# Optimization experiments

Measured on AMD Instinct MI355X. Metric: run time of the kernel, lower is better.

The kernel has to match this reference:

```python
import jax, jax.numpy as jnp
import numpy as np
import math

B, S, D = 4, 2048, 1024
H = 1
HD = D // H  # head_dim == hidden_dim since num_heads=1 (required by source's phase_encoder Linear)
HALF = HD // 2
SYNC_LOSS_WEIGHT = 0.01


def setup_inputs() -> dict:
    key = jax.random.key(0)
    ks = jax.random.split(key, 11)
    wstd = 0.02
    inp = {
        "x": jax.random.normal(ks[0], (B, S, D), dtype=jnp.float32),
        "Wq": jax.random.normal(ks[1], (D, D), dtype=jnp.float32) * wstd,
        "bq": jnp.zeros((D,), jnp.float32),
        "Wk": jax.random.normal(ks[2], (D, D), dtype=jnp.float32) * wstd,
        "bk": jnp.zeros((D,), jnp.float32),
        "Wv": jax.random.normal(ks[3], (D, D), dtype=jnp.float32) * wstd,
        "bv": jnp.zeros((D,), jnp.float32),
        "Wp": jax.random.normal(ks[4], (D, D), dtype=jnp.float32) * wstd,
        "bp": jnp.zeros((D,), jnp.float32),
        "Wo": jax.random.normal(ks[5], (D, D), dtype=jnp.float32) * wstd,
        "bo": jnp.zeros((D,), jnp.float32),
        "bifurcation_param": jnp.asarray(1.0, jnp.float32),
        "phase_coupling": jnp.asarray(0.5, jnp.float32),
    }
    return inp


def _phase(t, Wp, bp):
    # t: [B,H,S,HD] -> instantaneous phase via angle(complex(first_half, second_half))
    pf = t @ Wp.T + bp
    re, im = pf[..., :HALF], pf[..., HALF:]
    return jnp.arctan2(im, re)  # [B,H,S,HALF]


def reference(x, Wq, bq, Wk, bk, Wv, bv, Wp, bp, Wo, bo, bifurcation_param, phase_coupling):
    b, s, d = x.shape
    Q = (x @ Wq.T + bq).reshape(b, s, H, HD).transpose(0, 2, 1, 3)  # [B,H,S,HD]
    K = (x @ Wk.T + bk).reshape(b, s, H, HD).transpose(0, 2, 1, 3)
    V = (x @ Wv.T + bv).reshape(b, s, H, HD).transpose(0, 2, 1, 3)

    scores = jnp.einsum("bhqd,bhkd->bhqk", Q, K) / math.sqrt(HD)

    pQ = _phase(Q, Wp, bp)
    pK = _phase(K, Wp, bp)
    # mean_d cos(pQ - pK) == (cos(pQ)@cos(pK)^T + sin(pQ)@sin(pK)^T) / HALF
    sync = (jnp.einsum("bhqd,bhkd->bhqk", jnp.cos(pQ), jnp.cos(pK))
            + jnp.einsum("bhqd,bhkd->bhqk", jnp.sin(pQ), jnp.sin(pK))) / HALF

    t = jnp.tanh(scores)
    bif = bifurcation_param * t * (1.0 - t)

    chaotic = scores + phase_coupling * sync + bif
    attn = jax.nn.softmax(chaotic, axis=-1)

    av = jnp.einsum("bhqk,bhkd->bhqd", attn, V)
    av = av.transpose(0, 2, 1, 3).reshape(b, s, d)
    out = av @ Wo.T + bo

    # torch.var default: unbiased (ddof=1), over last dim of sync
    sync_loss = SYNC_LOSS_WEIGHT * jnp.var(sync, axis=-1, ddof=1).mean()
    return out, sync_loss
```

## Files before the change

### kernel.cpp

```cpp
#include <hip/hip_runtime.h>
#include <hip/hip_bf16.h>
#include <math.h>

#define S_LEN 2048
#define D_MODEL 1024
#define N_BATCH 4
#define N_HALF 512

typedef unsigned short u16;
typedef __attribute__((ext_vector_type(8))) short bf16x8;
typedef __attribute__((ext_vector_type(4))) float f32x4;

__device__ inline u16 f2bf(float v) {
  __hip_bfloat16 h = __float2bfloat16(v);
  return *reinterpret_cast<u16*>(&h);
}
__device__ inline float bf2f(u16 u) {
  __hip_bfloat16 h = *reinterpret_cast<__hip_bfloat16*>(&u);
  return __bfloat162float(h);
}
__device__ inline void gl2lds16(const void* g, void* l) {
  __builtin_amdgcn_global_load_lds(
      (const __attribute__((address_space(1))) unsigned int*)g,
      (__attribute__((address_space(3))) unsigned int*)l, 16, 0, 0);
}
__device__ inline float fast_tanh(float x) {
  float e = __expf(2.0f * x);
  return 1.0f - 2.0f / (e + 1.0f);
}

__global__ __launch_bounds__(256)
void cast_bf4(const float* __restrict__ src, u16* __restrict__ dst, long long n4) {
  long long i = (long long)blockIdx.x * 256 + threadIdx.x;
  if (i >= n4) return;
  float4 v = ((const float4*)src)[i];
  ushort4 o;
  o.x = f2bf(v.x); o.y = f2bf(v.y); o.z = f2bf(v.z); o.w = f2bf(v.w);
  ((ushort4*)dst)[i] = o;
}
__global__ __launch_bounds__(256)
void cast_split(const float* __restrict__ src, u16* __restrict__ hi,
                u16* __restrict__ lo, long long n) {
  long long i = (long long)blockIdx.x * 256 + threadIdx.x;
  if (i < n) {
    float v = src[i];
    u16 h = f2bf(v);
    hi[i] = h;
    lo[i] = f2bf(v - bf2f(h));
  }
}
__global__ __launch_bounds__(256)
void transpose_split(const float* __restrict__ src, u16* __restrict__ hi,
                     u16* __restrict__ lo) {
  __shared__ float t[32][33];
  const int bx = blockIdx.x * 32;
  const int by = blockIdx.y * 32;
  const int c = threadIdx.x & 31;
  const int r0 = (threadIdx.x >> 5) * 4;
#pragma unroll
  for (int r = 0; r < 4; r++)
    t[r0 + r][c] = src[(long long)(by + r0 + r) * D_MODEL + bx + c];
  __syncthreads();
#pragma unroll
  for (int r = 0; r < 4; r++) {
    float v = t[c][r0 + r];
    long long idx = (long long)(bx + r0 + r) * D_MODEL + by + c;
    u16 h = f2bf(v);
    hi[idx] = h;
    lo[idx] = f2bf(v - bf2f(h));
  }
}
__global__ __launch_bounds__(256)
void zero_stats(float* __restrict__ p, int n) {
  int i = blockIdx.x * 256 + threadIdx.x;
  if (i < n) p[i] = 0.f;
}
__global__ __launch_bounds__(256)
void w2_bias(const float* __restrict__ Wo, const float* __restrict__ bv,
             float* __restrict__ w2b) {
  const int d = blockIdx.x;
  const int tid = threadIdx.x;
  float acc = 0.f;
  for (int j = tid; j < D_MODEL; j += 256)
    acc += Wo[(long long)d * D_MODEL + j] * bv[j];
#pragma unroll
  for (int m = 1; m < 64; m <<= 1) acc += __shfl_xor(acc, m);
  __shared__ float red[4];
  if ((tid & 63) == 0) red[tid >> 6] = acc;
  __syncthreads();
  if (tid == 0) w2b[d] = red[0] + red[1] + red[2] + red[3];
}

__global__ __launch_bounds__(256, 2)
void qk_fused(const u16* __restrict__ X, const u16* __restrict__ Wq,
              const u16* __restrict__ Wk,
              const float* __restrict__ bq, const float* __restrict__ bk,
              u16* __restrict__ Qo, u16* __restrict__ Ko) {
  __shared__ u16 Xs[128 * 32];
  __shared__ u16 Qs[128 * 32];
  __shared__ u16 Ks[128 * 32];
  const int tid  = threadIdx.x;
  const int wave = tid >> 6;
  const int lane = tid & 63;
  const int quad = lane >> 4;
  const int tc   = lane & 15;
  const int bm = blockIdx.y * 128;
  const int bn = blockIdx.x * 128;
  const int wm = (wave & 1) * 64;
  const int wn = (wave >> 1) * 64;

  f32x4 acc1[4][4], acc2[4][4];
#pragma unroll
  for (int i = 0; i < 4; i++)
#pragma unroll
    for (int j = 0; j < 4; j++) {
      acc1[i][j] = (f32x4){0.f, 0.f, 0.f, 0.f};
      acc2[i][j] = (f32x4){0.f, 0.f, 0.f, 0.f};
    }

  const int srow = wave * 32 + (lane >> 2);
  const int scol = (lane & 3) * 8;
  const u16* gx = X  + (long long)(bm + srow) * D_MODEL + scol;
  const u16* gq = Wq + (long long)(bn + srow) * D_MODEL + scol;
  const u16* gk = Wk + (long long)(bn + srow) * D_MODEL + scol;
  const int wb = (wave * 32) * 32;
  const long long r16 = 16LL * D_MODEL;

  for (int k0 = 0; k0 < D_MODEL; k0 += 32) {
    gl2lds16(gx,       Xs + wb);
    gl2lds16(gx + r16, Xs + wb + 512);
    gl2lds16(gq,       Qs + wb);
    gl2lds16(gq + r16, Qs + wb + 512);
    gl2lds16(gk,       Ks + wb);
    gl2lds16(gk + r16, Ks + wb + 512);
    gx += 32; gq += 32; gk += 32;
    __syncthreads();
    bf16x8 af[4], bq4[4], bk4[4];
#pragma unroll
    for (int i = 0; i < 4; i++)
      af[i] = *(const bf16x8*)(Xs + (wm + i * 16 + tc) * 32 + quad * 8);
#pragma unroll
    for (int j = 0; j < 4; j++) {
      int o = (wn + j * 16 + tc) * 32 + quad * 8;
      bq4[j] = *(const bf16x8*)(Qs + o);
      bk4[j] = *(const bf16x8*)(Ks + o);
    }
#pragma unroll
    for (int i = 0; i < 4; i++)
#pragma unroll
      for (int j = 0; j < 4; j++) {
        acc1[i][j] = __builtin_amdgcn_mfma_f32_16x16x32_bf16(af[i], bq4[j], acc1[i][j], 0, 0, 0);
        acc2[i][j] = __builtin_amdgcn_mfma_f32_16x16x32_bf16(af[i], bk4[j], acc2[i][j], 0, 0, 0);
      }
    __syncthreads();
  }

#pragma unroll
  for (int i = 0; i < 4; i++) {
    const int row0 = bm + wm + i * 16 + quad * 4;
#pragma unroll
    for (int j = 0; j < 4; j++) {
      const int col = bn + wn + j * 16 + tc;
#pragma unroll
      for (int r = 0; r < 4; r++) {
        long long idx = (long long)(row0 + r) * D_MODEL + col;
        Qo[idx] = f2bf(acc1[i][j][r] + bq[col]);
        Ko[idx] = f2bf(acc2[i][j][r] + bk[col]);
      }
    }
  }
}

__global__ __launch_bounds__(256, 2)
void pf_fused(const u16* __restrict__ Qb, const u16* __restrict__ Wp,
              const float* __restrict__ bp,
              u16* __restrict__ pfQ, u16* __restrict__ pfK,
              long long TDo) {
  __shared__ u16 Qs[128 * 32];
  __shared__ u16 Ks[128 * 32];
  __shared__ u16 Ws[128 * 32];
  const int tid  = threadIdx.x;
  const int wave = tid >> 6;
  const int lane = tid & 63;
  const int quad = lane >> 4;
  const int tc   = lane & 15;
  const int bm = blockIdx.y * 128;
  const int bn = blockIdx.x * 128;
  const int wm = (wave & 1) * 64;
  const int wn = (wave >> 1) * 64;

  f32x4 acc1[4][4], acc2[4][4];
#pragma unroll
  for (int i = 0; i < 4; i++)
#pragma unroll
    for (int j = 0; j < 4; j++) {
      acc1[i][j] = (f32x4){0.f, 0.f, 0.f, 0.f};
      acc2[i][j] = (f32x4){0.f, 0.f, 0.f, 0.f};
    }

  const int srow = wave * 32 + (lane >> 2);
  const int scol = (lane & 3) * 8;
  const u16* gq = Qb + (long long)(bm + srow) * D_MODEL + scol;
  const u16* gk = gq + TDo;
  const u16* gw = Wp + (long long)(bn + srow) * D_MODEL + scol;
  const int wb = (wave * 32) * 32;
  const long long r16 = 16LL * D_MODEL;

  for (int k0 = 0; k0 < D_MODEL; k0 += 32) {
    gl2lds16(gq,       Qs + wb);
    gl2lds16(gq + r16, Qs + wb + 512);
    gl2lds16(gk,       Ks + wb);
    gl2lds16(gk + r16, Ks + wb + 512);
    gl2lds16(gw,       Ws + wb);
    gl2lds16(gw + r16, Ws + wb + 512);
    gq += 32; gk += 32; gw += 32;
    __syncthreads();
    bf16x8 aq[4], ak[4], bw[4];
#pragma unroll
    for (int i = 0; i < 4; i++) {
      int o = (wm + i * 16 + tc) * 32 + quad * 8;
      aq[i] = *(const bf16x8*)(Qs + o);
      ak[i] = *(const bf16x8*)(Ks + o);
    }
#pragma unroll
    for (int j = 0; j < 4; j++)
      bw[j] = *(const bf16x8*)(Ws + (wn + j * 16 + tc) * 32 + quad * 8);
#pragma unroll
    for (int i = 0; i < 4; i++)
#pragma unroll
      for (int j = 0; j < 4; j++) {
        acc1[i][j] = __builtin_amdgcn_mfma_f32_16x16x32_bf16(aq[i], bw[j], acc1[i][j], 0, 0, 0);
        acc2[i][j] = __builtin_amdgcn_mfma_f32_16x16x32_bf16(ak[i], bw[j], acc2[i][j], 0, 0, 0);
      }
    __syncthreads();
  }

#pragma unroll
  for (int i = 0; i < 4; i++) {
    const int row0 = bm + wm + i * 16 + quad * 4;
#pragma unroll
    for (int j = 0; j < 4; j++) {
      const int col = bn + wn + j * 16 + tc;
#pragma unroll
      for (int r = 0; r < 4; r++) {
        long long idx = (long long)(row0 + r) * D_MODEL + col;
        float b = bp[col];
        pfQ[idx] = f2bf(acc1[i][j][r] + b);
        pfK[idx] = f2bf(acc2[i][j][r] + b);
      }
    }
  }
}

__global__ __launch_bounds__(256)
void mfma_gemm_out3(const u16* __restrict__ Ah, const u16* __restrict__ Al,
                    const u16* __restrict__ Bh, const u16* __restrict__ Bl,
                    const float* __restrict__ bias, float* __restrict__ C,
                    int N, int K) {
  __shared__ u16 Ash[128 * 32];
  __shared__ u16 Asl[128 * 32];
  __shared__ u16 Bsh[128 * 32];
  __shared__ u16 Bsl[128 * 32];
  const int tid  = threadIdx.x;
  const int wave = tid >> 6;
  const int lane = tid & 63;
  const int quad = lane >> 4;
  const int tc   = lane & 15;
  const int bm = blockIdx.y * 128;
  const int bn = blockIdx.x * 128;
  const int wm = (wave & 1) * 64;
  const int wn = (wave >> 1) * 64;

  f32x4 acc[4][4];
#pragma unroll
  for (int i = 0; i < 4; i++)
#pragma unroll
    for (int j = 0; j < 4; j++) acc[i][j] = (f32x4){0.f, 0.f, 0.f, 0.f};

  const int srow = wave * 32 + (lane >> 2);
  const int scol = (lane & 3) * 8;
  long long aoff = (long long)(bm + srow) * K + scol;
  long long boff = (long long)(bn + srow) * K + scol;
  const u16 *gah = Ah + aoff, *gal = Al + aoff;
  const u16 *gbh = Bh + boff, *gbl = Bl + boff;
  const int wbase = (wave * 32) * 32;
  const long long r16K = 16LL * K;

  for (int k0 = 0; k0 < K; k0 += 32) {
    gl2lds16(gah,        Ash + wbase);
    gl2lds16(gah + r16K, Ash + wbase + 512);
    gl2lds16(gal,        Asl + wbase);
    gl2lds16(gal + r16K, Asl + wbase + 512);
    gl2lds16(gbh,        Bsh + wbase);
    gl2lds16(gbh + r16K, Bsh + wbase + 512);
    gl2lds16(gbl,        Bsl + wbase);
    gl2lds16(gbl + r16K, Bsl + wbase + 512);
    gah += 32; gal += 32; gbh += 32; gbl += 32;
    __syncthreads();
    bf16x8 ah[4], al[4], bh[4], bl[4];
#pragma unroll
    for (int i = 0; i < 4; i++) {
      int o = (wm + i * 16 + tc) * 32 + quad * 8;
      ah[i] = *(const bf16x8*)(Ash + o);
      al[i] = *(const bf16x8*)(Asl + o);
    }
#pragma unroll
    for (int j = 0; j < 4; j++) {
      int o = (wn + j * 16 + tc) * 32 + quad * 8;
      bh[j] = *(const bf16x8*)(Bsh + o);
      bl[j] = *(const bf16x8*)(Bsl + o);
    }
#pragma unroll
    for (int i = 0; i < 4; i++)
#pragma unroll
      for (int j = 0; j < 4; j++) {
        acc[i][j] = __builtin_amdgcn_mfma_f32_16x16x32_bf16(ah[i], bh[j], acc[i][j], 0, 0, 0);
        acc[i][j] = __builtin_amdgcn_mfma_f32_16x16x32_bf16(ah[i], bl[j], acc[i][j], 0, 0, 0);
        acc[i][j] = __builtin_amdgcn_mfma_f32_16x16x32_bf16(al[i], bh[j], acc[i][j], 0, 0, 0);
      }
    __syncthreads();
  }
#pragma unroll
  for (int i = 0; i < 4; i++) {
    const int row0 = bm + wm + i * 16 + quad * 4;
#pragma unroll
    for (int j = 0; j < 4; j++) {
      const int col = bn + wn + j * 16 + tc;
      float b = bias ? bias[col] : 0.f;
#pragma unroll
      for (int r = 0; r < 4; r++)
        C[(long long)(row0 + r) * N + col] = acc[i][j][r] + b;
    }
  }
}

__global__ __launch_bounds__(256)
void vwt_kernel(const u16* __restrict__ W2h, const u16* __restrict__ W2l,
                const u16* __restrict__ X, const float* __restrict__ w2b,
                u16* __restrict__ Ch, u16* __restrict__ Cl,
                long long sB, long long sC) {
  __shared__ u16 Ah[128 * 32];
  __shared__ u16 Al[128 * 32];
  __shared__ u16 Bs[128 * 32];
  const int tid  = threadIdx.x;
  const int wave = tid >> 6;
  const int lane = tid & 63;
  const int quad = lane >> 4;
  const int tc   = lane & 15;
  const int bm = blockIdx.y * 128;
  const int bn = blockIdx.x * 128;
  const long long z = blockIdx.z;
  const int wm = (wave & 1) * 64;
  const int wn = (wave >> 1) * 64;

  f32x4 acc[4][4];
#pragma unroll
  for (int i = 0; i < 4; i++)
#pragma unroll
    for (int j = 0; j < 4; j++) acc[i][j] = (f32x4){0.f, 0.f, 0.f, 0.f};

  const int srow = wave * 32 + (lane >> 2);
  const int scol = (lane & 3) * 8;
  const long long aoff = (long long)(bm + srow) * D_MODEL + scol;
  const u16* gah = W2h + aoff;
  const u16* gal = W2l + aoff;
  const u16* gb  = X + z * sB + (long long)(bn + srow) * D_MODEL + scol;
  const int wb = (wave * 32) * 32;
  const long long r16 = 16LL * D_MODEL;

  for (int k0 = 0; k0 < D_MODEL; k0 += 32) {
    gl2lds16(gah,       Ah + wb);
    gl2lds16(gah + r16, Ah + wb + 512);
    gl2lds16(gal,       Al + wb);
    gl2lds16(gal + r16, Al + wb + 512);
    gl2lds16(gb,        Bs + wb);
    gl2lds16(gb + r16,  Bs + wb + 512);
    gah += 32; gal += 32; gb += 32;
    __syncthreads();
    bf16x8 ah4[4], al4[4], bx[4];
#pragma unroll
    for (int i = 0; i < 4; i++) {
      int o = (wm + i * 16 + tc) * 32 + quad * 8;
      ah4[i] = *(const bf16x8*)(Ah + o);
      al4[i] = *(const bf16x8*)(Al + o);
    }
#pragma unroll
    for (int j = 0; j < 4; j++)
      bx[j] = *(const bf16x8*)(Bs + (wn + j * 16 + tc) * 32 + quad * 8);
#pragma unroll
    for (int i = 0; i < 4; i++)
#pragma unroll
      for (int j = 0; j < 4; j++) {
        acc[i][j] = __builtin_amdgcn_mfma_f32_16x16x32_bf16(ah4[i], bx[j], acc[i][j], 0, 0, 0);
        acc[i][j] = __builtin_amdgcn_mfma_f32_16x16x32_bf16(al4[i], bx[j], acc[i][j], 0, 0, 0);
      }
    __syncthreads();
  }

  u16* Chz = Ch + z * sC;
  u16* Clz = Cl + z * sC;
#pragma unroll
  for (int i = 0; i < 4; i++) {
    const int row0 = bm + wm + i * 16 + quad * 4;
#pragma unroll
    for (int j = 0; j < 4; j++) {
      const int col = bn + wn + j * 16 + tc;
#pragma unroll
      for (int r = 0; r < 4; r++) {
        float v = acc[i][j][r] + w2b[row0 + r];
        long long idx = (long long)(row0 + r) * S_LEN + col;
        u16 h = f2bf(v);
        Chz[idx] = h;
        Clz[idx] = f2bf(v - bf2f(h));
      }
    }
  }
}

__global__ __launch_bounds__(256)
void gemm_bsplit(const u16* __restrict__ A,
                 const u16* __restrict__ Bh, const u16* __restrict__ Bl,
                 const float* __restrict__ bias, float* __restrict__ C,
                 int N, int K, long long sA, long long sB, long long sC) {
  __shared__ u16 As[128 * 32];
  __shared__ u16 Bsh[128 * 32];
  __shared__ u16 Bsl[128 * 32];
  const int tid  = threadIdx.x;
  const int wave = tid >> 6;
  const int lane = tid & 63;
  const int quad = lane >> 4;
  const int tc   = lane & 15;
  const int bm = blockIdx.y * 128;
  const int bn = blockIdx.x * 128;
  const long long z = blockIdx.z;
  const int wm = (wave & 1) * 64;
  const int wn = (wave >> 1) * 64;

  f32x4 acc[4][4];
#pragma unroll
  for (int i = 0; i < 4; i++)
#pragma unroll
    for (int j = 0; j < 4; j++) acc[i][j] = (f32x4){0.f, 0.f, 0.f, 0.f};

  const int srow = wave * 32 + (lane >> 2);
  const int scol = (lane & 3) * 8;
  const long long boff = (long long)(bn + srow) * K + scol;
  const u16* ga  = A + z * sA + (long long)(bm + srow) * K + scol;
  const u16* gbh = Bh + z * sB + boff;
  const u16* gbl = Bl + z * sB + boff;
  const int wb = (wave * 32) * 32;
  const long long r16K = 16LL * K;

  for (int k0 = 0; k0 < K; k0 += 32) {
    gl2lds16(ga,         As + wb);
    gl2lds16(ga + r16K,  As + wb + 512);
    gl2lds16(gbh,        Bsh + wb);
    gl2lds16(gbh + r16K, Bsh + wb + 512);
    gl2lds16(gbl,        Bsl + wb);
    gl2lds16(gbl + r16K, Bsl + wb + 512);
    ga += 32; gbh += 32; gbl += 32;
    __syncthreads();
    bf16x8 af[4], bh[4], bl[4];
#pragma unroll
    for (int i = 0; i < 4; i++)
      af[i] = *(const bf16x8*)(As + (wm + i * 16 + tc) * 32 + quad * 8);
#pragma unroll
    for (int j = 0; j < 4; j++) {
      int o = (wn + j * 16 + tc) * 32 + quad * 8;
      bh[j] = *(const bf16x8*)(Bsh + o);
      bl[j] = *(const bf16x8*)(Bsl + o);
    }
#pragma unroll
    for (int i = 0; i < 4; i++)
#pragma unroll
      for (int j = 0; j < 4; j++) {
        acc[i][j] = __builtin_amdgcn_mfma_f32_16x16x32_bf16(af[i], bh[j], acc[i][j], 0, 0, 0);
        acc[i][j] = __builtin_amdgcn_mfma_f32_16x16x32_bf16(af[i], bl[j], acc[i][j], 0, 0, 0);
      }
    __syncthreads();
  }

  float* Cz = C + z * sC;
#pragma unroll
  for (int i = 0; i < 4; i++) {
    const int row0 = bm + wm + i * 16 + quad * 4;
#pragma unroll
    for (int j = 0; j < 4; j++) {
      const int col = bn + wn + j * 16 + tc;
#pragma unroll
      for (int r = 0; r < 4; r++)
        Cz[(long long)(row0 + r) * N + col] = acc[i][j][r] + bias[col];
    }
  }
}

__global__ __launch_bounds__(256, 2)
void chaotic_fused(const u16* __restrict__ Q, const u16* __restrict__ Kt,
                   const u16* __restrict__ Uq, const u16* __restrict__ Uk,
                   float* __restrict__ Cc,
                   float* __restrict__ ssum, float* __restrict__ ssq,
                   const float* __restrict__ bifp, const float* __restrict__ pcp) {
  __shared__ u16 Qs[128 * 64];
  __shared__ u16 Ks[128 * 64];
  __shared__ u16 Us[128 * 64];
  __shared__ u16 Ws[128 * 64];
  const int tid  = threadIdx.x;
  const int wave = tid >> 6;
  const int lane = tid & 63;
  const int quad = lane >> 4;
  const int tc   = lane & 15;
  const int bm = blockIdx.y * 128;
  const int bn = blockIdx.x * 128;
  const long long z = blockIdx.z;
  const long long sQ = (long long)S_LEN * D_MODEL;
  const int wm = (wave & 1) * 64;
  const int wn = (wave >> 1) * 64;

  f32x4 acc1[4][4], acc2[4][4];
#pragma unroll
  for (int i = 0; i < 4; i++)
#pragma unroll
    for (int j = 0; j < 4; j++) {
      acc1[i][j] = (f32x4){0.f, 0.f, 0.f, 0.f};
      acc2[i][j] = (f32x4){0.f, 0.f, 0.f, 0.f};
    }

  const int srow8  = lane >> 3;
  const int scol   = ((lane & 7) ^ srow8) * 8;
  const int srowb  = wave * 32;
  const u16* gq = Q  + z * sQ + (long long)(bm + srowb + srow8) * D_MODEL + scol;
  const u16* gk = Kt + z * sQ + (long long)(bn + srowb + srow8) * D_MODEL + scol;
  const u16* gu = Uq + z * sQ + (long long)(bm + srowb + srow8) * D_MODEL + scol;
  const u16* gw = Uk + z * sQ + (long long)(bn + srowb + srow8) * D_MODEL + scol;
  const int wb = srowb * 64;
  const long long r8 = 8LL * D_MODEL;

  const int swzA = tc & 7;

  for (int k0 = 0; k0 < D_MODEL; k0 += 64) {
#pragma unroll
    for (int c = 0; c < 4; c++) {
      gl2lds16(gq + c * r8, Qs + wb + c * 512);
      gl2lds16(gk + c * r8, Ks + wb + c * 512);
      gl2lds16(gu + c * r8, Us + wb + c * 512);
      gl2lds16(gw + c * r8, Ws + wb + c * 512);
    }
    gq += 64; gk += 64; gu += 64; gw += 64;
    __syncthreads();
    {
      bf16x8 af[4][2], bg[4][2];
#pragma unroll
      for (int i = 0; i < 4; i++) {
        const int ra = (wm + i * 16 + tc) * 64;
        const int rb = (wn + i * 16 + tc) * 64;
#pragma unroll
        for (int ks = 0; ks < 2; ks++) {
          const int co = ((ks * 4 + quad) ^ swzA) * 8;
          af[i][ks] = *(const bf16x8*)(Qs + ra + co);
          bg[i][ks] = *(const bf16x8*)(Ks + rb + co);
        }
      }
#pragma unroll
      for (int i = 0; i < 4; i++)
#pragma unroll
        for (int j = 0; j < 4; j++) {
          acc1[i][j] = __builtin_amdgcn_mfma_f32_16x16x32_bf16(af[i][0], bg[j][0], acc1[i][j], 0, 0, 0);
          acc1[i][j] = __builtin_amdgcn_mfma_f32_16x16x32_bf16(af[i][1], bg[j][1], acc1[i][j], 0, 0, 0);
        }
    }
    {
      bf16x8 cf[4][2], dg[4][2];
#pragma unroll
      for (int i = 0; i < 4; i++) {
        const int ra = (wm + i * 16 + tc) * 64;
        const int rb = (wn + i * 16 + tc) * 64;
#pragma unroll
        for (int ks = 0; ks < 2; ks++) {
          const int co = ((ks * 4 + quad) ^ swzA) * 8;
          cf[i][ks] = *(const bf16x8*)(Us + ra + co);
          dg[i][ks] = *(const bf16x8*)(Ws + rb + co);
        }
      }
#pragma unroll
      for (int i = 0; i < 4; i++)
#pragma unroll
        for (int j = 0; j < 4; j++) {
          acc2[i][j] = __builtin_amdgcn_mfma_f32_16x16x32_bf16(cf[i][0], dg[j][0], acc2[i][j], 0, 0, 0);
          acc2[i][j] = __builtin_amdgcn_mfma_f32_16x16x32_bf16(cf[i][1], dg[j][1], acc2[i][j], 0, 0, 0);
        }
    }
    __syncthreads();
  }

  const float bif = *bifp;
  const float pc  = *pcp;
  float rsum[4][4], rsq[4][4];
#pragma unroll
  for (int i = 0; i < 4; i++)
#pragma unroll
    for (int r = 0; r < 4; r++) { rsum[i][r] = 0.f; rsq[i][r] = 0.f; }

  float* C = Cc + z * (long long)S_LEN * S_LEN;
#pragma unroll
  for (int i = 0; i < 4; i++) {
    const int row0 = bm + wm + i * 16 + quad * 4;
#pragma unroll
    for (int j = 0; j < 4; j++) {
      const int col = bn + wn + j * 16 + tc;
#pragma unroll
      for (int r = 0; r < 4; r++) {
        float sc = acc1[i][j][r] * 0.03125f;
        float sy = acc2[i][j][r] * (1.0f / 512.0f);
        float t  = fast_tanh(sc);
        C[(long long)(row0 + r) * S_LEN + col] = sc + pc * sy + bif * t * (1.0f - t);
        rsum[i][r] += sy;
        rsq[i][r]  += sy * sy;
      }
    }
  }
#pragma unroll
  for (int m = 1; m < 16; m <<= 1) {
#pragma unroll
    for (int i = 0; i < 4; i++)
#pragma unroll
      for (int r = 0; r < 4; r++) {
        rsum[i][r] += __shfl_xor(rsum[i][r], m);
        rsq[i][r]  += __shfl_xor(rsq[i][r], m);
      }
  }
  if (tc == 0) {
#pragma unroll
    for (int i = 0; i < 4; i++)
#pragma unroll
      for (int r = 0; r < 4; r++) {
        long long rr = z * S_LEN + bm + wm + i * 16 + quad * 4 + r;
        atomicAdd(&ssum[rr], rsum[i][r]);
        atomicAdd(&ssq[rr],  rsq[i][r]);
      }
  }
}

__global__ __launch_bounds__(256)
void phase_norm_bf(u16* __restrict__ U, long long n_rows) {
  long long idx = (long long)blockIdx.x * 256 + threadIdx.x;
  if (idx >= n_rows * 64) return;
  long long row = idx >> 6;
  int j0 = (int)(idx & 63) * 8;
  u16* p = U + row * D_MODEL + j0;
  bf16x8 re8 = *(const bf16x8*)p;
  bf16x8 im8 = *(const bf16x8*)(p + N_HALF);
  bf16x8 ro, io;
#pragma unroll
  for (int i = 0; i < 8; i++) {
    float re = bf2f((u16)re8[i]);
    float im = bf2f((u16)im8[i]);
    float n2 = re * re + im * im;
    float cr = 1.f, sr = 0.f;
    if (n2 > 0.f) {
      float inv = 1.0f / sqrtf(n2);
      cr = re * inv; sr = im * inv;
    }
    ro[i] = (short)f2bf(cr);
    io[i] = (short)f2bf(sr);
  }
  *(bf16x8*)p = ro;
  *(bf16x8*)(p + N_HALF) = io;
}

__global__ __launch_bounds__(256)
void softmax_bf(const float* __restrict__ Cc, u16* __restrict__ P) {
  const long long row = (long long)blockIdx.y * S_LEN + blockIdx.x;
  const float* p = Cc + row * S_LEN;
  u16* q = P + row * S_LEN;
  const int tid = threadIdx.x;
  float v[8];
  float m = -3.402823466e+38f;
#pragma unroll
  for (int i = 0; i < 8; i++) { v[i] = p[tid + i * 256]; m = fmaxf(m, v[i]); }
#pragma unroll
  for (int mask = 1; mask < 64; mask <<= 1) m = fmaxf(m, __shfl_xor(m, mask));
  __shared__ float red[8];
  if ((tid & 63) == 0) red[tid >> 6] = m;
  __syncthreads();
  m = fmaxf(fmaxf(red[0], red[1]), fmaxf(red[2], red[3]));
  float s = 0.f;
#pragma unroll
  for (int i = 0; i < 8; i++) { v[i] = __expf(v[i] - m); s += v[i]; }
#pragma unroll
  for (int mask = 1; mask < 64; mask <<= 1) s += __shfl_xor(s, mask);
  __syncthreads();
  if ((tid & 63) == 0) red[4 + (tid >> 6)] = s;
  __syncthreads();
  s = red[4] + red[5] + red[6] + red[7];
  float inv = 1.0f / s;
#pragma unroll
  for (int i = 0; i < 8; i++) q[tid + i * 256] = f2bf(v[i] * inv);
}

__global__ __launch_bounds__(1024)
void syncloss_kernel(const float* __restrict__ ssum, const float* __restrict__ ssq,
                     float* __restrict__ out) {
  const int tid = threadIdx.x;
  float acc = 0.f;
  for (int r = tid; r < N_BATCH * S_LEN; r += 1024) {
    float su = ssum[r], sq = ssq[r];
    acc += (sq - su * su * (1.0f / 2048.0f)) * (1.0f / 2047.0f);
  }
#pragma unroll
  for (int mask = 1; mask < 64; mask <<= 1) acc += __shfl_xor(acc, mask);
  __shared__ float red[16];
  if ((tid & 63) == 0) red[tid >> 6] = acc;
  __syncthreads();
  if (tid == 0) {
    float t = 0.f;
#pragma unroll
    for (int k = 0; k < 16; k++) t += red[k];
    out[0] = 0.01f * (t / (float)(N_BATCH * S_LEN));
  }
}

extern "C" void kernel_launch(void* const* d_in, const int* in_sizes, int n_in,
                              void* d_out, int out_size, void* d_ws, size_t ws_size,
                              hipStream_t stream) {
  const float* x    = (const float*)d_in[0];
  const float* Wq   = (const float*)d_in[1];
  const float* bq   = (const float*)d_in[2];
  const float* Wk   = (const float*)d_in[3];
  const float* bk   = (const float*)d_in[4];
  const float* Wv   = (const float*)d_in[5];
  const float* bv   = (const float*)d_in[6];
  const float* Wp   = (const float*)d_in[7];
  const float* bp   = (const float*)d_in[8];
  const float* Wo   = (const float*)d_in[9];
  const float* bo   = (const float*)d_in[10];
  const float* bifp = (const float*)d_in[11];
  const float* pcp  = (const float*)d_in[12];
  float* out = (float*)d_out;

  const long long NROW = (long long)N_BATCH * S_LEN;
  const long long TD   = NROW * D_MODEL;
  const long long WSZ  = (long long)D_MODEL * D_MODEL;

  u16* xbf   = (u16*)d_ws;
  u16* wqb   = xbf + TD;
  u16* wkb   = wqb + WSZ;
  u16* wpb   = wkb + WSZ;
  u16* woh   = wpb + WSZ;
  u16* wol   = woh + WSZ;
  u16* wvth  = wol + WSZ;
  u16* wvtl  = wvth + WSZ;
  u16* w2h   = wvtl + WSZ;
  u16* w2l   = w2h + WSZ;
  float* W2f = (float*)(w2l + WSZ);
  float* w2b = W2f + WSZ;
  u16* Qbf   = (u16*)(w2b + D_MODEL);
  u16* Kbf   = Qbf + TD;
  u16* pfQ   = Kbf + TD;
  u16* pfK   = pfQ + TD;
  float* Cc  = (float*)(pfK + TD);
  float* ssum = Cc + (long long)N_BATCH * S_LEN * S_LEN;
  float* ssq  = ssum + NROW;
  u16* attn = Qbf;
  u16* vwh  = pfQ;
  u16* vwl  = pfK;

  dim3 blk(256);
  const long long sQ = (long long)S_LEN * D_MODEL;
  const long long sS = (long long)S_LEN * S_LEN;

  cast_bf4<<<(int)(TD / 4 / 256), blk, 0, stream>>>(x, xbf, TD / 4);
  cast_bf4<<<(int)(WSZ / 4 / 256), blk, 0, stream>>>(Wq, wqb, WSZ / 4);
  cast_bf4<<<(int)(WSZ / 4 / 256), blk, 0, stream>>>(Wk, wkb, WSZ / 4);
  cast_bf4<<<(int)(WSZ / 4 / 256), blk, 0, stream>>>(Wp, wpb, WSZ / 4);
  cast_split<<<(int)(WSZ / 256), blk, 0, stream>>>(Wo, woh, wol, WSZ);
  transpose_split<<<dim3(32, 32), blk, 0, stream>>>(Wv, wvth, wvtl);
  mfma_gemm_out3<<<dim3(8, 8, 1), blk, 0, stream>>>(
      woh, wol, wvth, wvtl, nullptr, W2f, D_MODEL, D_MODEL);
  cast_split<<<(int)(WSZ / 256), blk, 0, stream>>>(W2f, w2h, w2l, WSZ);
  w2_bias<<<D_MODEL, blk, 0, stream>>>(Wo, bv, w2b);

  qk_fused<<<dim3(8, 64), blk, 0, stream>>>(xbf, wqb, wkb, bq, bk, Qbf, Kbf);
  pf_fused<<<dim3(8, 64), blk, 0, stream>>>(Qbf, wpb, bp, pfQ, pfK, TD);
  phase_norm_bf<<<(int)(2 * NROW * 64 / 256), blk, 0, stream>>>(pfQ, 2 * NROW);
  zero_stats<<<(int)((2 * NROW + 255) / 256), blk, 0, stream>>>(ssum, (int)(2 * NROW));

  chaotic_fused<<<dim3(16, 16, N_BATCH), blk, 0, stream>>>(
      Qbf, Kbf, pfQ, pfK, Cc, ssum, ssq, bifp, pcp);
  vwt_kernel<<<dim3(16, 8, N_BATCH), blk, 0, stream>>>(
      w2h, w2l, xbf, w2b, vwh, vwl, sQ, sQ);
  softmax_bf<<<dim3(S_LEN, N_BATCH), blk, 0, stream>>>(Cc, attn);
  gemm_bsplit<<<dim3(8, 16, N_BATCH), blk, 0, stream>>>(
      attn, vwh, vwl, bo, out,
      D_MODEL, S_LEN, sS, sQ, sQ);
  syncloss_kernel<<<1, 1024, 0, stream>>>(ssum, ssq, out + TD);
}
```

Before: 507.3 us.

## Double K-tile depth to 64 with XOR-swizzled LDS layout in all GEMMs

Every bf16 MFMA GEMM kernel now stages a 128x64 K-slice per iteration instead of 128x32. This halves the number of barrier pairs and loop iterations. An XOR swizzle on the 16-byte column chunk is applied both on the global-to-LDS load and on the fragment reads, to avoid LDS bank conflicts from the 128-byte row stride. LDS use per block doubles, which may limit occupancy for the kernels that hold four tiles, and register pressure rises because twice as many fragments are held per iteration.

```diff
diff --git a/kernel.cpp b/kernel.cpp
--- a/kernel.cpp
+++ b/kernel.cpp
@@ -91,14 +91,15 @@
   if (tid == 0) w2b[d] = red[0] + red[1] + red[2] + red[3];
 }
 
+
 __global__ __launch_bounds__(256, 2)
 void qk_fused(const u16* __restrict__ X, const u16* __restrict__ Wq,
               const u16* __restrict__ Wk,
               const float* __restrict__ bq, const float* __restrict__ bk,
               u16* __restrict__ Qo, u16* __restrict__ Ko) {
-  __shared__ u16 Xs[128 * 32];
-  __shared__ u16 Qs[128 * 32];
-  __shared__ u16 Ks[128 * 32];
+  __shared__ u16 Xs[128 * 64];
+  __shared__ u16 Qs[128 * 64];
+  __shared__ u16 Ks[128 * 64];
   const int tid  = threadIdx.x;
   const int wave = tid >> 6;
   const int lane = tid & 63;
@@ -118,39 +119,46 @@
       acc2[i][j] = (f32x4){0.f, 0.f, 0.f, 0.f};
     }
 
-  const int srow = wave * 32 + (lane >> 2);
-  const int scol = (lane & 3) * 8;
-  const u16* gx = X  + (long long)(bm + srow) * D_MODEL + scol;
-  const u16* gq = Wq + (long long)(bn + srow) * D_MODEL + scol;
-  const u16* gk = Wk + (long long)(bn + srow) * D_MODEL + scol;
-  const int wb = (wave * 32) * 32;
-  const long long r16 = 16LL * D_MODEL;
-
-  for (int k0 = 0; k0 < D_MODEL; k0 += 32) {
-    gl2lds16(gx,       Xs + wb);
-    gl2lds16(gx + r16, Xs + wb + 512);
-    gl2lds16(gq,       Qs + wb);
-    gl2lds16(gq + r16, Qs + wb + 512);
-    gl2lds16(gk,       Ks + wb);
-    gl2lds16(gk + r16, Ks + wb + 512);
-    gx += 32; gq += 32; gk += 32;
-    __syncthreads();
-    bf16x8 af[4], bq4[4], bk4[4];
+  const int srow8 = lane >> 3;
+  const int scol  = ((lane & 7) ^ srow8) * 8;
+  const int srowb = wave * 32;
+  const u16* gx = X  + (long long)(bm + srowb + srow8) * D_MODEL + scol;
+  const u16* gq = Wq + (long long)(bn + srowb + srow8) * D_MODEL + scol;
+  const u16* gk = Wk + (long long)(bn + srowb + srow8) * D_MODEL + scol;
+  const int wb = srowb * 64;
+  const long long r8 = 8LL * D_MODEL;
+  const int swzA = tc & 7;
+
+  for (int k0 = 0; k0 < D_MODEL; k0 += 64) {
+#pragma unroll
+    for (int c = 0; c < 4; c++) {
+      gl2lds16(gx + c * r8, Xs + wb + c * 512);
+      gl2lds16(gq + c * r8, Qs + wb + c * 512);
+      gl2lds16(gk + c * r8, Ks + wb + c * 512);
+    }
+    gx += 64; gq += 64; gk += 64;
+    __syncthreads();
+    bf16x8 af[4][2], bq4[4][2], bk4[4][2];
+#pragma unroll
+    for (int i = 0; i < 4; i++) {
+      const int ra = (wm + i * 16 + tc) * 64;
+      const int rb = (wn + i * 16 + tc) * 64;
+#pragma unroll
+      for (int ks = 0; ks < 2; ks++) {
+        const int co = ((ks * 4 + quad) ^ swzA) * 8;
+        af[i][ks]  = *(const bf16x8*)(Xs + ra + co);
+        bq4[i][ks] = *(const bf16x8*)(Qs + rb + co);
+        bk4[i][ks] = *(const bf16x8*)(Ks + rb + co);
+      }
+    }
 #pragma unroll
     for (int i = 0; i < 4; i++)
-      af[i] = *(const bf16x8*)(Xs + (wm + i * 16 + tc) * 32 + quad * 8);
-#pragma unroll
-    for (int j = 0; j < 4; j++) {
-      int o = (wn + j * 16 + tc) * 32 + quad * 8;
-      bq4[j] = *(const bf16x8*)(Qs + o);
-      bk4[j] = *(const bf16x8*)(Ks + o);
-    }
-#pragma unroll
-    for (int i = 0; i < 4; i++)
 #pragma unroll
       for (int j = 0; j < 4; j++) {
-        acc1[i][j] = __builtin_amdgcn_mfma_f32_16x16x32_bf16(af[i], bq4[j], acc1[i][j], 0, 0, 0);
-        acc2[i][j] = __builtin_amdgcn_mfma_f32_16x16x32_bf16(af[i], bk4[j], acc2[i][j], 0, 0, 0);
+        acc1[i][j] = __builtin_amdgcn_mfma_f32_16x16x32_bf16(af[i][0], bq4[j][0], acc1[i][j], 0, 0, 0);
+        acc2[i][j] = __builtin_amdgcn_mfma_f32_16x16x32_bf16(af[i][0], bk4[j][0], acc2[i][j], 0, 0, 0);
+        acc1[i][j] = __builtin_amdgcn_mfma_f32_16x16x32_bf16(af[i][1], bq4[j][1], acc1[i][j], 0, 0, 0);
+        acc2[i][j] = __builtin_amdgcn_mfma_f32_16x16x32_bf16(af[i][1], bk4[j][1], acc2[i][j], 0, 0, 0);
       }
     __syncthreads();
   }
@@ -176,9 +184,9 @@
               const float* __restrict__ bp,
               u16* __restrict__ pfQ, u16* __restrict__ pfK,
               long long TDo) {
-  __shared__ u16 Qs[128 * 32];
-  __shared__ u16 Ks[128 * 32];
-  __shared__ u16 Ws[128 * 32];
+  __shared__ u16 Qs[128 * 64];
+  __shared__ u16 Ks[128 * 64];
+  __shared__ u16 Ws[128 * 64];
   const int tid  = threadIdx.x;
   const int wave = tid >> 6;
   const int lane = tid & 63;
@@ -198,39 +206,46 @@
       acc2[i][j] = (f32x4){0.f, 0.f, 0.f, 0.f};
     }
 
-  const int srow = wave * 32 + (lane >> 2);
-  const int scol = (lane & 3) * 8;
-  const u16* gq = Qb + (long long)(bm + srow) * D_MODEL + scol;
+  const int srow8 = lane >> 3;
+  const int scol  = ((lane & 7) ^ srow8) * 8;
+  const int srowb = wave * 32;
+  const u16* gq = Qb + (long long)(bm + srowb + srow8) * D_MODEL + scol;
   const u16* gk = gq + TDo;
-  const u16* gw = Wp + (long long)(bn + srow) * D_MODEL + scol;
-  const int wb = (wave * 32) * 32;
-  const long long r16 = 16LL * D_MODEL;
-
-  for (int k0 = 0; k0 < D_MODEL; k0 += 32) {
-    gl2lds16(gq,       Qs + wb);
-    gl2lds16(gq + r16, Qs + wb + 512);
-    gl2lds16(gk,       Ks + wb);
-    gl2lds16(gk + r16, Ks + wb + 512);
-    gl2lds16(gw,       Ws + wb);
-    gl2lds16(gw + r16, Ws + wb + 512);
-    gq += 32; gk += 32; gw += 32;
-    __syncthreads();
-    bf16x8 aq[4], ak[4], bw[4];
+  const u16* gw = Wp + (long long)(bn + srowb + srow8) * D_MODEL + scol;
+  const int wb = srowb * 64;
+  const long long r8 = 8LL * D_MODEL;
+  const int swzA = tc & 7;
+
+  for (int k0 = 0; k0 < D_MODEL; k0 += 64) {
+#pragma unroll
+    for (int c = 0; c < 4; c++) {
+      gl2lds16(gq + c * r8, Qs + wb + c * 512);
+      gl2lds16(gk + c * r8, Ks + wb + c * 512);
+      gl2lds16(gw + c * r8, Ws + wb + c * 512);
+    }
+    gq += 64; gk += 64; gw += 64;
+    __syncthreads();
+    bf16x8 aq[4][2], ak[4][2], bw[4][2];
 #pragma unroll
     for (int i = 0; i < 4; i++) {
-      int o = (wm + i * 16 + tc) * 32 + quad * 8;
-      aq[i] = *(const bf16x8*)(Qs + o);
-      ak[i] = *(const bf16x8*)(Ks + o);
-    }
-#pragma unroll
-    for (int j = 0; j < 4; j++)
-      bw[j] = *(const bf16x8*)(Ws + (wn + j * 16 + tc) * 32 + quad * 8);
+      const int ra = (wm + i * 16 + tc) * 64;
+      const int rb = (wn + i * 16 + tc) * 64;
+#pragma unroll
+      for (int ks = 0; ks < 2; ks++) {
+        const int co = ((ks * 4 + quad) ^ swzA) * 8;
+        aq[i][ks] = *(const bf16x8*)(Qs + ra + co);
+        ak[i][ks] = *(const bf16x8*)(Ks + ra + co);
+        bw[i][ks] = *(const bf16x8*)(Ws + rb + co);
+      }
+    }
 #pragma unroll
     for (int i = 0; i < 4; i++)
 #pragma unroll
       for (int j = 0; j < 4; j++) {
-        acc1[i][j] = __builtin_amdgcn_mfma_f32_16x16x32_bf16(aq[i], bw[j], acc1[i][j], 0, 0, 0);
-        acc2[i][j] = __builtin_amdgcn_mfma_f32_16x16x32_bf16(ak[i], bw[j], acc2[i][j], 0, 0, 0);
+        acc1[i][j] = __builtin_amdgcn_mfma_f32_16x16x32_bf16(aq[i][0], bw[j][0], acc1[i][j], 0, 0, 0);
+        acc2[i][j] = __builtin_amdgcn_mfma_f32_16x16x32_bf16(ak[i][0], bw[j][0], acc2[i][j], 0, 0, 0);
+        acc1[i][j] = __builtin_amdgcn_mfma_f32_16x16x32_bf16(aq[i][1], bw[j][1], acc1[i][j], 0, 0, 0);
+        acc2[i][j] = __builtin_amdgcn_mfma_f32_16x16x32_bf16(ak[i][1], bw[j][1], acc2[i][j], 0, 0, 0);
       }
     __syncthreads();
   }
@@ -257,10 +272,10 @@
                     const u16* __restrict__ Bh, const u16* __restrict__ Bl,
                     const float* __restrict__ bias, float* __restrict__ C,
                     int N, int K) {
-  __shared__ u16 Ash[128 * 32];
-  __shared__ u16 Asl[128 * 32];
-  __shared__ u16 Bsh[128 * 32];
-  __shared__ u16 Bsl[128 * 32];
+  __shared__ u16 Ash[128 * 64];
+  __shared__ u16 Asl[128 * 64];
+  __shared__ u16 Bsh[128 * 64];
+  __shared__ u16 Bsl[128 * 64];
   const int tid  = threadIdx.x;
   const int wave = tid >> 6;
   const int lane = tid & 63;
@@ -277,46 +292,51 @@
 #pragma unroll
     for (int j = 0; j < 4; j++) acc[i][j] = (f32x4){0.f, 0.f, 0.f, 0.f};
 
-  const int srow = wave * 32 + (lane >> 2);
-  const int scol = (lane & 3) * 8;
-  long long aoff = (long long)(bm + srow) * K + scol;
-  long long boff = (long long)(bn + srow) * K + scol;
+  const int srow8 = lane >> 3;
+  const int scol  = ((lane & 7) ^ srow8) * 8;
+  const int srowb = wave * 32;
+  long long aoff = (long long)(bm + srowb + srow8) * K + scol;
+  long long boff = (long long)(bn + srowb + srow8) * K + scol;
   const u16 *gah = Ah + aoff, *gal = Al + aoff;
   const u16 *gbh = Bh + boff, *gbl = Bl + boff;
-  const int wbase = (wave * 32) * 32;
-  const long long r16K = 16LL * K;
-
-  for (int k0 = 0; k0 < K; k0 += 32) {
-    gl2lds16(gah,        Ash + wbase);
-    gl2lds16(gah + r16K, Ash + wbase + 512);
-    gl2lds16(gal,        Asl + wbase);
-    gl2lds16(gal + r16K, Asl + wbase + 512);
-    gl2lds16(gbh,        Bsh + wbase);
-    gl2lds16(gbh + r16K, Bsh + wbase + 512);
-    gl2lds16(gbl,        Bsl + wbase);
-    gl2lds16(gbl + r16K, Bsl + wbase + 512);
-    gah += 32; gal += 32; gbh += 32; gbl += 32;
-    __syncthreads();
-    bf16x8 ah[4], al[4], bh[4], bl[4];
+  const int wb = srowb * 64;
+  const long long r8K = 8LL * K;
+  const int swzA = tc & 7;
+
+  for (int k0 = 0; k0 < K; k0 += 64) {
+#pragma unroll
+    for (int c = 0; c < 4; c++) {
+      gl2lds16(gah + c * r8K, Ash + wb + c * 512);
+      gl2lds16(gal + c * r8K, Asl + wb + c * 512);
+      gl2lds16(gbh + c * r8K, Bsh + wb + c * 512);
+      gl2lds16(gbl + c * r8K, Bsl + wb + c * 512);
+    }
+    gah += 64; gal += 64; gbh += 64; gbl += 64;
+    __syncthreads();
+    bf16x8 ah[4][2], al[4][2], bh[4][2], bl[4][2];
 #pragma unroll
     for (int i = 0; i < 4; i++) {
-      int o = (wm + i * 16 + tc) * 32 + quad * 8;
-      ah[i] = *(const bf16x8*)(Ash + o);
-      al[i] = *(const bf16x8*)(Asl + o);
-    }
-#pragma unroll
-    for (int j = 0; j < 4; j++) {
-      int o = (wn + j * 16 + tc) * 32 + quad * 8;
-      bh[j] = *(const bf16x8*)(Bsh + o);
-      bl[j] = *(const bf16x8*)(Bsl + o);
+      const int ra = (wm + i * 16 + tc) * 64;
+      const int rb = (wn + i * 16 + tc) * 64;
+#pragma unroll
+      for (int ks = 0; ks < 2; ks++) {
+        const int co = ((ks * 4 + quad) ^ swzA) * 8;
+        ah[i][ks] = *(const bf16x8*)(Ash + ra + co);
+        al[i][ks] = *(const bf16x8*)(Asl + ra + co);
+        bh[i][ks] = *(const bf16x8*)(Bsh + rb + co);
+        bl[i][ks] = *(const bf16x8*)(Bsl + rb + co);
+      }
     }
 #pragma unroll
     for (int i = 0; i < 4; i++)
 #pragma unroll
       for (int j = 0; j < 4; j++) {
-        acc[i][j] = __builtin_amdgcn_mfma_f32_16x16x32_bf16(ah[i], bh[j], acc[i][j], 0, 0, 0);
-        acc[i][j] = __builtin_amdgcn_mfma_f32_16x16x32_bf16(ah[i], bl[j], acc[i][j], 0, 0, 0);
-        acc[i][j] = __builtin_amdgcn_mfma_f32_16x16x32_bf16(al[i], bh[j], acc[i][j], 0, 0, 0);
+#pragma unroll
+        for (int ks = 0; ks < 2; ks++) {
+          acc[i][j] = __builtin_amdgcn_mfma_f32_16x16x32_bf16(ah[i][ks], bh[j][ks], acc[i][j], 0, 0, 0);
+          acc[i][j] = __builtin_amdgcn_mfma_f32_16x16x32_bf16(ah[i][ks], bl[j][ks], acc[i][j], 0, 0, 0);
+          acc[i][j] = __builtin_amdgcn_mfma_f32_16x16x32_bf16(al[i][ks], bh[j][ks], acc[i][j], 0, 0, 0);
+        }
       }
     __syncthreads();
   }
@@ -339,9 +359,9 @@
                 const u16* __restrict__ X, const float* __restrict__ w2b,
                 u16* __restrict__ Ch, u16* __restrict__ Cl,
                 long long sB, long long sC) {
-  __shared__ u16 Ah[128 * 32];
-  __shared__ u16 Al[128 * 32];
-  __shared__ u16 Bs[128 * 32];
+  __shared__ u16 Ah[128 * 64];
+  __shared__ u16 Al[128 * 64];
+  __shared__ u16 Bs[128 * 64];
   const int tid  = threadIdx.x;
   const int wave = tid >> 6;
   const int lane = tid & 63;
@@ -359,40 +379,47 @@
 #pragma unroll
     for (int j = 0; j < 4; j++) acc[i][j] = (f32x4){0.f, 0.f, 0.f, 0.f};
 
-  const int srow = wave * 32 + (lane >> 2);
-  const int scol = (lane & 3) * 8;
-  const long long aoff = (long long)(bm + srow) * D_MODEL + scol;
+  const int srow8 = lane >> 3;
+  const int scol  = ((lane & 7) ^ srow8) * 8;
+  const int srowb = wave * 32;
+  const long long aoff = (long long)(bm + srowb + srow8) * D_MODEL + scol;
   const u16* gah = W2h + aoff;
   const u16* gal = W2l + aoff;
-  const u16* gb  = X + z * sB + (long long)(bn + srow) * D_MODEL + scol;
-  const int wb = (wave * 32) * 32;
-  const long long r16 = 16LL * D_MODEL;
-
-  for (int k0 = 0; k0 < D_MODEL; k0 += 32) {
-    gl2lds16(gah,       Ah + wb);
-    gl2lds16(gah + r16, Ah + wb + 512);
-    gl2lds16(gal,       Al + wb);
-    gl2lds16(gal + r16, Al + wb + 512);
-    gl2lds16(gb,        Bs + wb);
-    gl2lds16(gb + r16,  Bs + wb + 512);
-    gah += 32; gal += 32; gb += 32;
-    __syncthreads();
-    bf16x8 ah4[4], al4[4], bx[4];
+  const u16* gb  = X + z * sB + (long long)(bn + srowb + srow8) * D_MODEL + scol;
+  const int wb = srowb * 64;
+  const long long r8 = 8LL * D_MODEL;
+  const int swzA = tc & 7;
+
+  for (int k0 = 0; k0 < D_MODEL; k0 += 64) {
+#pragma unroll
+    for (int c = 0; c < 4; c++) {
+      gl2lds16(gah + c * r8, Ah + wb + c * 512);
+      gl2lds16(gal + c * r8, Al + wb + c * 512);
+      gl2lds16(gb  + c * r8, Bs + wb + c * 512);
+    }
+    gah += 64; gal += 64; gb += 64;
+    __syncthreads();
+    bf16x8 ah4[4][2], al4[4][2], bx[4][2];
 #pragma unroll
     for (int i = 0; i < 4; i++) {
-      int o = (wm + i * 16 + tc) * 32 + quad * 8;
-      ah4[i] = *(const bf16x8*)(Ah + o);
-      al4[i] = *(const bf16x8*)(Al + o);
-    }
-#pragma unroll
-    for (int j = 0; j < 4; j++)
-      bx[j] = *(const bf16x8*)(Bs + (wn + j * 16 + tc) * 32 + quad * 8);
+      const int ra = (wm + i * 16 + tc) * 64;
+      const int rb = (wn + i * 16 + tc) * 64;
+#pragma unroll
+      for (int ks = 0; ks < 2; ks++) {
+        const int co = ((ks * 4 + quad) ^ swzA) * 8;
+        ah4[i][ks] = *(const bf16x8*)(Ah + ra + co);
+        al4[i][ks] = *(const bf16x8*)(Al + ra + co);
+        bx[i][ks]  = *(const bf16x8*)(Bs + rb + co);
+      }
+    }
 #pragma unroll
     for (int i = 0; i < 4; i++)
 #pragma unroll
       for (int j = 0; j < 4; j++) {
-        acc[i][j] = __builtin_amdgcn_mfma_f32_16x16x32_bf16(ah4[i], bx[j], acc[i][j], 0, 0, 0);
-        acc[i][j] = __builtin_amdgcn_mfma_f32_16x16x32_bf16(al4[i], bx[j], acc[i][j], 0, 0, 0);
+        acc[i][j] = __builtin_amdgcn_mfma_f32_16x16x32_bf16(ah4[i][0], bx[j][0], acc[i][j], 0, 0, 0);
+        acc[i][j] = __builtin_amdgcn_mfma_f32_16x16x32_bf16(al4[i][0], bx[j][0], acc[i][j], 0, 0, 0);
+        acc[i][j] = __builtin_amdgcn_mfma_f32_16x16x32_bf16(ah4[i][1], bx[j][1], acc[i][j], 0, 0, 0);
+        acc[i][j] = __builtin_amdgcn_mfma_f32_16x16x32_bf16(al4[i][1], bx[j][1], acc[i][j], 0, 0, 0);
       }
     __syncthreads();
   }
@@ -422,9 +449,9 @@
                  const u16* __restrict__ Bh, const u16* __restrict__ Bl,
                  const float* __restrict__ bias, float* __restrict__ C,
                  int N, int K, long long sA, long long sB, long long sC) {
-  __shared__ u16 As[128 * 32];
-  __shared__ u16 Bsh[128 * 32];
-  __shared__ u16 Bsl[128 * 32];
+  __shared__ u16 As[128 * 64];
+  __shared__ u16 Bsh[128 * 64];
+  __shared__ u16 Bsl[128 * 64];
   const int tid  = threadIdx.x;
   const int wave = tid >> 6;
   const int lane = tid & 63;
@@ -442,40 +469,47 @@
 #pragma unroll
     for (int j = 0; j < 4; j++) acc[i][j] = (f32x4){0.f, 0.f, 0.f, 0.f};
 
-  const int srow = wave * 32 + (lane >> 2);
-  const int scol = (lane & 3) * 8;
-  const long long boff = (long long)(bn + srow) * K + scol;
-  const u16* ga  = A + z * sA + (long long)(bm + srow) * K + scol;
+  const int srow8 = lane >> 3;
+  const int scol  = ((lane & 7) ^ srow8) * 8;
+  const int srowb = wave * 32;
+  const long long boff = (long long)(bn + srowb + srow8) * K + scol;
+  const u16* ga  = A + z * sA + (long long)(bm + srowb + srow8) * K + scol;
   const u16* gbh = Bh + z * sB + boff;
   const u16* gbl = Bl + z * sB + boff;
-  const int wb = (wave * 32) * 32;
-  const long long r16K = 16LL * K;
-
-  for (int k0 = 0; k0 < K; k0 += 32) {
-    gl2lds16(ga,         As + wb);
-    gl2lds16(ga + r16K,  As + wb + 512);
-    gl2lds16(gbh,        Bsh + wb);
-    gl2lds16(gbh + r16K, Bsh + wb + 512);
-    gl2lds16(gbl,        Bsl + wb);
-    gl2lds16(gbl + r16K, Bsl + wb + 512);
-    ga += 32; gbh += 32; gbl += 32;
-    __syncthreads();
-    bf16x8 af[4], bh[4], bl[4];
+  const int wb = srowb * 64;
+  const long long r8K = 8LL * K;
+  const int swzA = tc & 7;
+
+  for (int k0 = 0; k0 < K; k0 += 64) {
+#pragma unroll
+    for (int c = 0; c < 4; c++) {
+      gl2lds16(ga  + c * r8K, As  + wb + c * 512);
+      gl2lds16(gbh + c * r8K, Bsh + wb + c * 512);
+      gl2lds16(gbl + c * r8K, Bsl + wb + c * 512);
+    }
+    ga += 64; gbh += 64; gbl += 64;
+    __syncthreads();
+    bf16x8 af[4][2], bh[4][2], bl[4][2];
+#pragma unroll
+    for (int i = 0; i < 4; i++) {
+      const int ra = (wm + i * 16 + tc) * 64;
+      const int rb = (wn + i * 16 + tc) * 64;
+#pragma unroll
+      for (int ks = 0; ks < 2; ks++) {
+        const int co = ((ks * 4 + quad) ^ swzA) * 8;
+        af[i][ks] = *(const bf16x8*)(As  + ra + co);
+        bh[i][ks] = *(const bf16x8*)(Bsh + rb + co);
+        bl[i][ks] = *(const bf16x8*)(Bsl + rb + co);
+      }
+    }
 #pragma unroll
     for (int i = 0; i < 4; i++)
-      af[i] = *(const bf16x8*)(As + (wm + i * 16 + tc) * 32 + quad * 8);
-#pragma unroll
-    for (int j = 0; j < 4; j++) {
-      int o = (wn + j * 16 + tc) * 32 + quad * 8;
-      bh[j] = *(const bf16x8*)(Bsh + o);
-      bl[j] = *(const bf16x8*)(Bsl + o);
-    }
-#pragma unroll
-    for (int i = 0; i < 4; i++)
 #pragma unroll
       for (int j = 0; j < 4; j++) {
-        acc[i][j] = __builtin_amdgcn_mfma_f32_16x16x32_bf16(af[i], bh[j], acc[i][j], 0, 0, 0);
-        acc[i][j] = __builtin_amdgcn_mfma_f32_16x16x32_bf16(af[i], bl[j], acc[i][j], 0, 0, 0);
+        acc[i][j] = __builtin_amdgcn_mfma_f32_16x16x32_bf16(af[i][0], bh[j][0], acc[i][j], 0, 0, 0);
+        acc[i][j] = __builtin_amdgcn_mfma_f32_16x16x32_bf16(af[i][0], bl[j][0], acc[i][j], 0, 0, 0);
+        acc[i][j] = __builtin_amdgcn_mfma_f32_16x16x32_bf16(af[i][1], bh[j][1], acc[i][j], 0, 0, 0);
+        acc[i][j] = __builtin_amdgcn_mfma_f32_16x16x32_bf16(af[i][1], bl[j][1], acc[i][j], 0, 0, 0);
       }
     __syncthreads();
   }
```

Measured after the change: 488.3 us. 3.8% less time.
